# Kernel optimization log

Measured on AMD Instinct MI355X. Metric: run time of the kernel, lower is better.

The kernel has to match this reference:

```python
import jax, jax.numpy as jnp
import numpy as np

N = 100000   # nodes
E = 1600000  # edges
F_IN = 128
H = 64
C = 40


def setup_inputs() -> dict:
    key = jax.random.key(0)
    ks = jax.random.split(key, 4)
    x = jax.random.normal(ks[0], (N, F_IN), dtype=jnp.float32)
    edge_index = jax.random.randint(ks[1], (2, E), 0, N, dtype=jnp.int64)
    # Glorot-ish init for weights, zero bias (PyG GCNConv default bias init is zeros)
    W1 = jax.random.normal(ks[2], (F_IN, H), dtype=jnp.float32) / np.float32(np.sqrt(F_IN))
    b1 = jnp.zeros((H,), jnp.float32)
    W2 = jax.random.normal(ks[3], (H, C), dtype=jnp.float32) / np.float32(np.sqrt(H))
    b2 = jnp.zeros((C,), jnp.float32)
    return {"x": x, "edge_index": edge_index, "W1": W1, "b1": b1, "W2": W2, "b2": b2}


def gcn_conv(x, W, b, src, dst):
    """GCNConv: D^-1/2 (A + I) D^-1/2 (x W) + b, edges flow src -> dst."""
    h = x @ W                                   # [N, out] transform first (out <= in)
    loop = jnp.arange(N, dtype=src.dtype)
    s = jnp.concatenate([src, loop])            # add self-loops
    d = jnp.concatenate([dst, loop])
    deg = jax.ops.segment_sum(jnp.ones_like(d, dtype=h.dtype), d, num_segments=N)
    dinv = jnp.where(deg > 0, jax.lax.rsqrt(deg), jnp.zeros_like(deg))
    norm = dinv[s] * dinv[d]                    # [E+N]
    msgs = h[s] * norm[:, None]                 # gather + scale
    out = jax.ops.segment_sum(msgs, d, num_segments=N)  # scatter-add
    return out + b


def reference(x, edge_index, W1, b1, W2, b2):
    src, dst = edge_index[0], edge_index[1]
    h = jax.nn.relu(gcn_conv(x, W1, b1, src, dst))   # dropout is identity in eval
    out = gcn_conv(h, W2, b2, src, dst)
    return jax.nn.log_softmax(out, axis=1)
```

## Files before the change

### kernel.cpp

```cpp
#include <hip/hip_runtime.h>

#define NN 100000
#define EE 1600000
#define FIN 128
#define HH 64
#define CC 40
#define NB 98
#define TR 64


__global__ void k_count(const int* __restrict__ dst, int* __restrict__ rp) {
  int e = blockIdx.x * blockDim.x + threadIdx.x;
  if (e < EE) atomicAdd(&rp[1 + dst[e]], 1);
}

__global__ void __launch_bounds__(1024)
k_scan_a(int* __restrict__ rp, float* __restrict__ dinv, int* __restrict__ bsum) {
  __shared__ int sm[1024];
  int i = blockIdx.x * 1024 + threadIdx.x;
  int c = (i < NN) ? rp[i + 1] : 0;
  if (i < NN) dinv[i] = rsqrtf((float)(c + 1));
  sm[threadIdx.x] = c;
  __syncthreads();
#pragma unroll
  for (int off = 1; off < 1024; off <<= 1) {
    int v = (threadIdx.x >= off) ? sm[threadIdx.x - off] : 0;
    __syncthreads();
    sm[threadIdx.x] += v;
    __syncthreads();
  }
  if (i < NN) rp[i + 1] = sm[threadIdx.x];
  if (threadIdx.x == 1023) bsum[blockIdx.x] = sm[1023];
}

__global__ void __launch_bounds__(128)
k_scan_b(int* __restrict__ bsum) {
  __shared__ int sm[128];
  int v = (threadIdx.x < NB) ? bsum[threadIdx.x] : 0;
  sm[threadIdx.x] = v;
  __syncthreads();
#pragma unroll
  for (int off = 1; off < 128; off <<= 1) {
    int u = (threadIdx.x >= off) ? sm[threadIdx.x - off] : 0;
    __syncthreads();
    sm[threadIdx.x] += u;
    __syncthreads();
  }
  bsum[threadIdx.x] = sm[threadIdx.x] - v;
}

__global__ void k_scan_c(int* __restrict__ rp, const int* __restrict__ bsum) {
  int i = blockIdx.x * blockDim.x + threadIdx.x;
  if (i < NN) rp[i + 1] += bsum[i >> 10];
}

__global__ void k_fill(const int* __restrict__ ei, int* __restrict__ wp,
                       int* __restrict__ col) {
  int e = blockIdx.x * blockDim.x + threadIdx.x;
  if (e < EE) {
    int s = ei[e];
    int d = ei[EE + e];
    int pos = atomicAdd(&wp[d], 1);
    col[pos] = s;
  }
}


__global__ void __launch_bounds__(256)
k_gemm1(const float* __restrict__ x, const float* __restrict__ W,
        const float* __restrict__ dinv, float* __restrict__ hs) {
  __shared__ float xs[TR * FIN];
  const int tid  = threadIdx.x;
  const int lane = tid & 63;
  const int wq   = tid >> 6;
  int base = blockIdx.x * TR;
  int rows = NN - base; if (rows > TR) rows = TR;

  {
    const float4* xg = reinterpret_cast<const float4*>(x + (size_t)base * FIN);
    float4* xsv = reinterpret_cast<float4*>(xs);
    int n4 = rows * (FIN / 4);
    for (int i = tid; i < n4; i += 256) xsv[i] = xg[i];
  }
  __syncthreads();

  const int r0 = wq * 16;
  float acc[16];
#pragma unroll
  for (int r = 0; r < 16; ++r) acc[r] = 0.f;

  for (int kc = 0; kc < 4; ++kc) {
    float wreg[32];
#pragma unroll
    for (int j = 0; j < 32; ++j) wreg[j] = W[(kc * 32 + j) * HH + lane];
#pragma unroll
    for (int r = 0; r < 16; ++r) {
      const float* xrow = &xs[(r0 + r) * FIN + kc * 32];
#pragma unroll
      for (int k4 = 0; k4 < 8; ++k4) {
        float4 xv = *reinterpret_cast<const float4*>(xrow + 4 * k4);
        acc[r] += xv.x * wreg[4 * k4 + 0];
        acc[r] += xv.y * wreg[4 * k4 + 1];
        acc[r] += xv.z * wreg[4 * k4 + 2];
        acc[r] += xv.w * wreg[4 * k4 + 3];
      }
    }
  }
#pragma unroll
  for (int r = 0; r < 16; ++r) {
    int row = base + r0 + r;
    if (r0 + r < rows) hs[(size_t)row * HH + lane] = acc[r] * dinv[row];
  }
}

__global__ void __launch_bounds__(256)
k_agg1(const int* __restrict__ rp, const int* __restrict__ col,
       const float* __restrict__ hs, const float* __restrict__ dinv,
       const float* __restrict__ b1, float* __restrict__ h1) {
  const int lane = threadIdx.x & 63;
  int d = blockIdx.x * 4 + (threadIdx.x >> 6);
  if (d >= NN) return;
  int e   = rp[d];
  int end = rp[d + 1];
  float acc = hs[(size_t)d * HH + lane];
  for (; e + 1 < end; e += 2) {
    int s0 = col[e], s1 = col[e + 1];
    acc += hs[(size_t)s0 * HH + lane];
    acc += hs[(size_t)s1 * HH + lane];
  }
  if (e < end) acc += hs[(size_t)col[e] * HH + lane];
  float v = acc * dinv[d] + b1[lane];
  h1[(size_t)d * HH + lane] = v > 0.f ? v : 0.f;
}

__global__ void __launch_bounds__(256)
k_gemm2(const float* __restrict__ h1, const float* __restrict__ W,
        const float* __restrict__ dinv, float* __restrict__ hs2) {
  __shared__ float xs[TR * HH];
  const int tid  = threadIdx.x;
  const int lane = tid & 63;
  const int wq   = tid >> 6;
  const int cl   = lane < CC ? lane : CC - 1;
  int base = blockIdx.x * TR;
  int rows = NN - base; if (rows > TR) rows = TR;

  {
    const float4* xg = reinterpret_cast<const float4*>(h1 + (size_t)base * HH);
    float4* xsv = reinterpret_cast<float4*>(xs);
    int n4 = rows * (HH / 4);
    for (int i = tid; i < n4; i += 256) xsv[i] = xg[i];
  }
  __syncthreads();

  const int r0 = wq * 16;
  float acc[16];
#pragma unroll
  for (int r = 0; r < 16; ++r) acc[r] = 0.f;

  for (int kc = 0; kc < 2; ++kc) {
    float wreg[32];
#pragma unroll
    for (int j = 0; j < 32; ++j) wreg[j] = W[(kc * 32 + j) * CC + cl];
#pragma unroll
    for (int r = 0; r < 16; ++r) {
      const float* xrow = &xs[(r0 + r) * HH + kc * 32];
#pragma unroll
      for (int k4 = 0; k4 < 8; ++k4) {
        float4 xv = *reinterpret_cast<const float4*>(xrow + 4 * k4);
        acc[r] += xv.x * wreg[4 * k4 + 0];
        acc[r] += xv.y * wreg[4 * k4 + 1];
        acc[r] += xv.z * wreg[4 * k4 + 2];
        acc[r] += xv.w * wreg[4 * k4 + 3];
      }
    }
  }
#pragma unroll
  for (int r = 0; r < 16; ++r) {
    int row = base + r0 + r;
    if (r0 + r < rows && lane < CC)
      hs2[(size_t)row * CC + lane] = acc[r] * dinv[row];
  }
}

__global__ void __launch_bounds__(256)
k_agg2(const int* __restrict__ rp, const int* __restrict__ col,
       const float* __restrict__ hs2, const float* __restrict__ dinv,
       const float* __restrict__ b2, float* __restrict__ out) {
  const int lane = threadIdx.x & 63;
  int d = blockIdx.x * 4 + (threadIdx.x >> 6);
  if (d >= NN) return;
  const bool act = lane < CC;
  int e   = rp[d];
  int end = rp[d + 1];
  float acc = act ? hs2[(size_t)d * CC + lane] : 0.f;
  for (; e + 1 < end; e += 2) {
    int s0 = col[e], s1 = col[e + 1];
    if (act) {
      acc += hs2[(size_t)s0 * CC + lane];
      acc += hs2[(size_t)s1 * CC + lane];
    }
  }
  if (e < end && act) acc += hs2[(size_t)col[e] * CC + lane];
  float v = act ? acc * dinv[d] + b2[lane] : -__builtin_inff();
  float m = v;
#pragma unroll
  for (int off = 32; off > 0; off >>= 1) m = fmaxf(m, __shfl_xor(m, off));
  float ex = act ? expf(v - m) : 0.f;
  float s = ex;
#pragma unroll
  for (int off = 32; off > 0; off >>= 1) s += __shfl_xor(s, off);
  if (act) out[(size_t)d * CC + lane] = v - m - logf(s);
}

extern "C" void kernel_launch(void* const* d_in, const int* in_sizes, int n_in,
                              void* d_out, int out_size, void* d_ws, size_t ws_size,
                              hipStream_t stream) {
  const float* x  = (const float*)d_in[0];
  const int*   ei = (const int*)d_in[1];
  const float* W1 = (const float*)d_in[2];
  const float* b1 = (const float*)d_in[3];
  const float* W2 = (const float*)d_in[4];
  const float* b2 = (const float*)d_in[5];
  float* out = (float*)d_out;

  float* dinv = (float*)d_ws;
  int*   rp   = (int*)(dinv + NN);
  int*   wp   = rp + NN + 1;
  int*   bsum = wp + NN;
  int*   col  = bsum + 128;
  float* hsA  = (float*)(col + EE);
  float* h1   = hsA + (size_t)NN * HH;

  hipMemsetAsync(rp, 0, (NN + 1) * sizeof(int), stream);

  k_count<<<(EE + 255) / 256, 256, 0, stream>>>(ei + EE, rp);
  k_scan_a<<<NB, 1024, 0, stream>>>(rp, dinv, bsum);
  k_scan_b<<<1, 128, 0, stream>>>(bsum);
  k_scan_c<<<(NN + 255) / 256, 256, 0, stream>>>(rp, bsum);
  hipMemcpyAsync(wp, rp, NN * sizeof(int), hipMemcpyDeviceToDevice, stream);
  k_fill<<<(EE + 255) / 256, 256, 0, stream>>>(ei, wp, col);

  int tiles = (NN + TR - 1) / TR;
  k_gemm1<<<tiles, 256, 0, stream>>>(x, W1, dinv, hsA);
  k_agg1<<<(NN + 3) / 4, 256, 0, stream>>>(rp, col, hsA, dinv, b1, h1);
  k_gemm2<<<tiles, 256, 0, stream>>>(h1, W2, dinv, hsA);
  k_agg2<<<(NN + 3) / 4, 256, 0, stream>>>(rp, col, hsA, dinv, b2, out);
}
```

Measured before the change: 587.7 us.

## Build CSR via two-pass bucketed partition with shared-memory atomics

Replaces the single-pass CSR fill, which did a global atomic per destination node, with two passes. The first pass groups edges into 128-node buckets using one global atomic per bucket and writes packed (local dst, src) words into the h1 buffer. The second pass gives each bucket its own block and scatters the edges into CSR slots using shared-memory atomics. This avoids the wp memcpy and scattered global atomics, at the cost of an extra pass over the edges and heavy contention on the 782 bucket counters.

After: 859.6 us. 1.46x slower.

```diff
diff --git a/kernel.cpp b/kernel.cpp
--- a/kernel.cpp
+++ b/kernel.cpp
@@ -7,6 +7,7 @@
 #define CC 40
 #define NB 98
 #define TR 64
+#define BKT 782
 
 
 __global__ void k_count(const int* __restrict__ dst, int* __restrict__ rp) {
@@ -54,14 +55,38 @@
   if (i < NN) rp[i + 1] += bsum[i >> 10];
 }
 
-__global__ void k_fill(const int* __restrict__ ei, int* __restrict__ wp,
-                       int* __restrict__ col) {
+__global__ void k_part(const int* __restrict__ ei, const int* __restrict__ rp,
+                       int* __restrict__ bcur, unsigned* __restrict__ part) {
   int e = blockIdx.x * blockDim.x + threadIdx.x;
   if (e < EE) {
     int s = ei[e];
     int d = ei[EE + e];
-    int pos = atomicAdd(&wp[d], 1);
-    col[pos] = s;
+    int b = d >> 7;
+    int pos = atomicAdd(&bcur[b], 1);
+    int base = rp[b << 7];
+    part[base + pos] = ((unsigned)(d & 127) << 17) | (unsigned)s;
+  }
+}
+
+__global__ void __launch_bounds__(256)
+k_fill2(const unsigned* __restrict__ part, const int* __restrict__ rp,
+        int* __restrict__ col) {
+  __shared__ int rpl[129];
+  __shared__ int cur[128];
+  int b  = blockIdx.x;
+  int nb = b << 7;
+  int nn = NN - nb; if (nn > 128) nn = 128;
+  for (int i = threadIdx.x; i < nn + 1; i += 256) rpl[i] = rp[nb + i];
+  for (int i = threadIdx.x; i < 128; i += 256) cur[i] = 0;
+  __syncthreads();
+  int e0 = rpl[0];
+  int e1 = rpl[nn];
+  for (int i = e0 + threadIdx.x; i < e1; i += 256) {
+    unsigned u = part[i];
+    int loc = (int)(u >> 17);
+    int s   = (int)(u & 0x1FFFFu);
+    int c = atomicAdd(&cur[loc], 1);
+    col[rpl[loc] + c] = s;
   }
 }
 
@@ -225,20 +250,21 @@
 
   float* dinv = (float*)d_ws;
   int*   rp   = (int*)(dinv + NN);
-  int*   wp   = rp + NN + 1;
-  int*   bsum = wp + NN;
+  int*   bcur = rp + NN + 1;
+  int*   bsum = bcur + BKT;
   int*   col  = bsum + 128;
   float* hsA  = (float*)(col + EE);
   float* h1   = hsA + (size_t)NN * HH;
-
-  hipMemsetAsync(rp, 0, (NN + 1) * sizeof(int), stream);
+  unsigned* part = (unsigned*)h1;
+
+  hipMemsetAsync(rp, 0, (NN + 1 + BKT) * sizeof(int), stream);
 
   k_count<<<(EE + 255) / 256, 256, 0, stream>>>(ei + EE, rp);
   k_scan_a<<<NB, 1024, 0, stream>>>(rp, dinv, bsum);
   k_scan_b<<<1, 128, 0, stream>>>(bsum);
   k_scan_c<<<(NN + 255) / 256, 256, 0, stream>>>(rp, bsum);
-  hipMemcpyAsync(wp, rp, NN * sizeof(int), hipMemcpyDeviceToDevice, stream);
-  k_fill<<<(EE + 255) / 256, 256, 0, stream>>>(ei, wp, col);
+  k_part<<<(EE + 255) / 256, 256, 0, stream>>>(ei, rp, bcur, part);
+  k_fill2<<<BKT, 256, 0, stream>>>(part, rp, col);
 
   int tiles = (NN + TR - 1) / TR;
   k_gemm1<<<tiles, 256, 0, stream>>>(x, W1, dinv, hsA);
```
